# Optimization experiments

Hardware: AMD Instinct MI355X
Metric: run time of the kernel (lower is better)

The kernel has to match this reference:

```python
import jax, jax.numpy as jnp
import numpy as np
from jax import lax

B, M, N = 4096, 306, 984
LAMBDA = 0.1
MAX_ITER = 50


def setup_inputs() -> dict:
    key = jax.random.key(0)
    k1, k2, k3, k4 = jax.random.split(key, 4)
    return {
        "r_real": jax.random.normal(k1, (B, M), dtype=jnp.float32),
        "r_imag": jax.random.normal(k2, (B, M), dtype=jnp.float32),
        # phi buffer: torch.randn(M, N, dtype=complex64) -> real/imag each ~N(0, 1/2)?
        # torch.randn(complex64) draws real & imag each from N(0, 1/sqrt(2)^2)=N(0,0.5).
        "phi_real": jax.random.normal(k3, (M, N), dtype=jnp.float32) * np.float32(1.0 / np.sqrt(2.0)),
        "phi_imag": jax.random.normal(k4, (M, N), dtype=jnp.float32) * np.float32(1.0 / np.sqrt(2.0)),
    }


def reference(r_real, r_imag, phi_real, phi_imag):
    phi = (phi_real + 1j * phi_imag).astype(jnp.complex64)          # [M, N]
    r = (r_real + 1j * r_imag).astype(jnp.complex64)                # [B, M]
    # step_size = 1 / ||phi||_2^2  (spectral norm squared)
    step = (1.0 / jnp.linalg.norm(phi, ord=2) ** 2).real.astype(jnp.float32)
    thresh = (LAMBDA * step).astype(jnp.float32)
    phi_c = jnp.conj(phi)

    def body(w, _):
        # error = w @ phi.T - r : [B, M]
        error = jnp.einsum("bn,mn->bm", w, phi) - r
        # gradient = error @ conj(phi) : [B, N]
        grad = jnp.einsum("bm,mn->bn", error, phi_c)
        w_next = w - step * grad
        w_mag = jnp.abs(w_next)
        new_mag = jax.nn.relu(w_mag - thresh)
        # polar(new_mag, angle(w_next))
        w_new = (new_mag * jnp.exp(1j * jnp.angle(w_next))).astype(jnp.complex64)
        return w_new, None

    w0 = jnp.zeros((r.shape[0], N), dtype=jnp.complex64)
    w, _ = lax.scan(body, w0, None, length=MAX_ITER)
    return jnp.abs(w).astype(jnp.float32)
```

## Files before the change

kernel.cpp:

```cpp
#include <hip/hip_runtime.h>
#include <math.h>

#define Bb 4096
#define Mm 306
#define Nn 984
#define NCP 1024
#define KA 2048
#define ITERS 50
#define KSQ 9

typedef _Float16 f16x8 __attribute__((ext_vector_type(8)));
typedef float f32x16 __attribute__((ext_vector_type(16)));

__device__ __forceinline__ void cmac(float2& c, const float2 a, const float2 b) {
    c.x = fmaf(a.x, b.x, c.x);
    c.x = fmaf(-a.y, b.y, c.x);
    c.y = fmaf(a.x, b.y, c.y);
    c.y = fmaf(a.y, b.x, c.y);
}

__device__ __forceinline__ unsigned short f16bits(float v) {
    union { _Float16 h; unsigned short u; } cv;
    cv.h = (_Float16)v;
    return cv.u;
}
__device__ __forceinline__ float f16lo(unsigned int u) {
    union { unsigned short s; _Float16 h; } cv; cv.s = (unsigned short)(u & 0xffffu);
    return (float)cv.h;
}
__device__ __forceinline__ float f16hi(unsigned int u) {
    union { unsigned short s; _Float16 h; } cv; cv.s = (unsigned short)(u >> 16);
    return (float)cv.h;
}

__device__ __forceinline__ void load_lds16(const void* g, void* l) {
    __builtin_amdgcn_global_load_lds((const __attribute__((address_space(1))) void*)g,
                                     (__attribute__((address_space(3))) void*)l, 16, 0, 0);
}

__device__ __forceinline__ size_t swzA(int b, int c) {
    return ((size_t)(((b >> 7) * 32 + (c >> 5)) * 1024 + ((c >> 2) & 7) * 128 + (b & 127))) * 4 + (c & 3);
}
__device__ __forceinline__ size_t swzB(int jr, int q) {
    return ((size_t)(((jr >> 7) * 32 + (q >> 5)) * 1024 + ((q >> 2) & 7) * 128 + (jr & 127))) * 4 + (q & 3);
}
__device__ __forceinline__ size_t swzA2(int b, int c) {
    return ((size_t)(((b >> 7) * 10 + (c >> 5)) * 1024 + ((c >> 2) & 7) * 128 + (b & 127))) * 4 + (c & 3);
}
__device__ __forceinline__ size_t swzB2(int jr, int q) {
    return ((size_t)(((jr >> 7) * 10 + (q >> 5)) * 1024 + ((q >> 2) & 7) * 128 + (jr & 127))) * 4 + (q & 3);
}

__global__ void gram_kernel(const float* __restrict__ pr, const float* __restrict__ pi,
                            float2* __restrict__ G) {
    __shared__ float2 As[32][33];
    __shared__ float2 Bs[32][33];
    int tx = threadIdx.x, ty = threadIdx.y;
    int t = ty * 16 + tx;
    int i0 = blockIdx.y * 32, j0 = blockIdx.x * 32;
    int zs = blockIdx.z * 246;
    int ze = zs + 246 < Nn ? zs + 246 : Nn;
    float2 acc[2][2] = {};
    for (int k0 = zs; k0 < ze; k0 += 32) {
        #pragma unroll
        for (int rep = 0; rep < 4; ++rep) {
            int idx = t + rep * 256;
            int rr = idx >> 5, cc = idx & 31;
            int gk = k0 + cc;
            int gi = i0 + rr, gj = j0 + rr;
            float2 a = make_float2(0.f, 0.f), b = make_float2(0.f, 0.f);
            if (gk < ze) {
                if (gi < Mm) a = make_float2(pr[(size_t)gi * Nn + gk], pi[(size_t)gi * Nn + gk]);
                if (gj < Mm) b = make_float2(pr[(size_t)gj * Nn + gk], pi[(size_t)gj * Nn + gk]);
            }
            As[rr][cc] = a; Bs[rr][cc] = b;
        }
        __syncthreads();
        #pragma unroll 8
        for (int kk = 0; kk < 32; ++kk) {
            float2 a0 = As[ty * 2][kk], a1 = As[ty * 2 + 1][kk];
            float2 b0 = Bs[tx * 2][kk], b1 = Bs[tx * 2 + 1][kk];
            #define GMAC(qq, aa, bb) \
                qq.x = fmaf(aa.x, bb.x, qq.x); qq.x = fmaf(aa.y, bb.y, qq.x); \
                qq.y = fmaf(aa.y, bb.x, qq.y); qq.y = fmaf(-aa.x, bb.y, qq.y);
            GMAC(acc[0][0], a0, b0) GMAC(acc[0][1], a0, b1)
            GMAC(acc[1][0], a1, b0) GMAC(acc[1][1], a1, b1)
            #undef GMAC
        }
        __syncthreads();
    }
    #pragma unroll
    for (int i = 0; i < 2; ++i) {
        int gi = i0 + ty * 2 + i;
        #pragma unroll
        for (int j = 0; j < 2; ++j) {
            int gj = j0 + tx * 2 + j;
            if (gi < Mm && gj < Mm) {
                atomicAdd(&G[gi * Mm + gj].x, acc[i][j].x);
                atomicAdd(&G[gi * Mm + gj].y, acc[i][j].y);
            }
        }
    }
}

__global__ void frob_kernel(const float2* __restrict__ H, float* __restrict__ slot, int n) {
    int idx = blockIdx.x * blockDim.x + threadIdx.x;
    int stride = gridDim.x * blockDim.x;
    float s = 0.f;
    for (int i = idx; i < n; i += stride) {
        float2 v = H[i];
        s = fmaf(v.x, v.x, s);
        s = fmaf(v.y, v.y, s);
    }
    #pragma unroll
    for (int o = 32; o > 0; o >>= 1) s += __shfl_down(s, o, 64);
    __shared__ float wsum[4];
    int lane = threadIdx.x & 63, wv = threadIdx.x >> 6;
    if (lane == 0) wsum[wv] = s;
    __syncthreads();
    if (threadIdx.x == 0) atomicAdd(slot, wsum[0] + wsum[1] + wsum[2] + wsum[3]);
}

__global__ void sqmm_kernel(const float2* __restrict__ A, float2* __restrict__ C,
                            const float* __restrict__ fslot) {
    __shared__ float2 As[32][33];
    __shared__ float2 Bs[32][33];
    float inv = 1.0f / fslot[0];
    int tx = threadIdx.x, ty = threadIdx.y;
    int t = ty * 16 + tx;
    int r0 = blockIdx.y * 32, c0 = blockIdx.x * 32;
    int zs = blockIdx.z * 80;
    int ze = zs + 80 < Mm ? zs + 80 : Mm;
    float2 acc[2][2] = {};
    for (int k0 = zs; k0 < ze; k0 += 32) {
        #pragma unroll
        for (int i = 0; i < 4; ++i) {
            int idx = t + i * 256;
            int rr = idx >> 5, cc = idx & 31;
            int gr = r0 + rr, gk = k0 + cc;
            As[rr][cc] = (gr < Mm && gk < ze) ? A[gr * Mm + gk] : make_float2(0.f, 0.f);
            int gk2 = k0 + rr, gc = c0 + cc;
            Bs[rr][cc] = (gk2 < ze && gc < Mm) ? A[gk2 * Mm + gc] : make_float2(0.f, 0.f);
        }
        __syncthreads();
        #pragma unroll 8
        for (int kk = 0; kk < 32; ++kk) {
            float2 a0 = As[ty * 2][kk], a1 = As[ty * 2 + 1][kk];
            float2 b0 = Bs[kk][tx * 2], b1 = Bs[kk][tx * 2 + 1];
            cmac(acc[0][0], a0, b0); cmac(acc[0][1], a0, b1);
            cmac(acc[1][0], a1, b0); cmac(acc[1][1], a1, b1);
        }
        __syncthreads();
    }
    #pragma unroll
    for (int i = 0; i < 2; ++i) {
        int gr = r0 + ty * 2 + i;
        #pragma unroll
        for (int j = 0; j < 2; ++j) {
            int gc = c0 + tx * 2 + j;
            if (gr < Mm && gc < Mm) {
                atomicAdd(&C[gr * Mm + gc].x, acc[i][j].x * inv);
                atomicAdd(&C[gr * Mm + gc].y, acc[i][j].y * inv);
            }
        }
    }
}

__global__ void rayleigh_kernel(const float2* __restrict__ H, const float2* __restrict__ G,
                                float* __restrict__ sc) {
    __shared__ float2 v[Mm];
    __shared__ float rn[320], rd[320];
    int t = threadIdx.x;
    if (t < Mm) {
        float2 s = make_float2(0.f, 0.f);
        for (int j = 0; j < Mm; ++j) { float2 h = H[t * Mm + j]; s.x += h.x; s.y += h.y; }
        v[t] = s;
    }
    __syncthreads();
    float num = 0.f, den = 0.f;
    if (t < Mm) {
        float2 u = make_float2(0.f, 0.f);
        for (int k = 0; k < Mm; ++k) {
            float2 g = G[k * Mm + t];
            float2 vk = v[k];
            u.x = fmaf(g.x, vk.x, u.x); u.x = fmaf(g.y, vk.y, u.x);
            u.y = fmaf(g.x, vk.y, u.y); u.y = fmaf(-g.y, vk.x, u.y);
        }
        float2 vt = v[t];
        num = vt.x * u.x + vt.y * u.y;
        den = vt.x * vt.x + vt.y * vt.y;
    }
    rn[t] = num; rd[t] = den;
    __syncthreads();
    if (t == 0) {
        float sn = 0.f, sd = 0.f;
        for (int i = 0; i < 320; ++i) { sn += rn[i]; sd += rd[i]; }
        float lam = sn / sd;
        float step = 1.0f / lam;
        sc[0] = step;
        sc[1] = 0.1f * step;
    }
}

__global__ void qpack_kernel(const float* __restrict__ pr, const float* __restrict__ pi,
                             unsigned int* __restrict__ Bu, const float* __restrict__ sc) {
    __shared__ float2 Pn[16][33];
    __shared__ float2 Pc[16][33];
    float nstep = -sc[0];
    int t = threadIdx.x;
    int tx = t & 15, ty = t >> 4;
    int n0 = blockIdx.x * 32, c0 = blockIdx.y * 32;
    float2 q[2][2] = {};
    for (int m0 = 0; m0 < Mm; m0 += 16) {
        #pragma unroll
        for (int rep = 0; rep < 2; ++rep) {
            int idx = t + rep * 256;
            int mm = idx >> 5, col = idx & 31;
            int gm = m0 + mm;
            float2 a = make_float2(0.f, 0.f), b = make_float2(0.f, 0.f);
            if (gm < Mm) {
                if (n0 + col < Nn) a = make_float2(pr[(size_t)gm * Nn + n0 + col], pi[(size_t)gm * Nn + n0 + col]);
                if (c0 + col < Nn) b = make_float2(pr[(size_t)gm * Nn + c0 + col], pi[(size_t)gm * Nn + c0 + col]);
            }
            Pn[mm][col] = a; Pc[mm][col] = b;
        }
        __syncthreads();
        #pragma unroll
        for (int mm = 0; mm < 16; ++mm) {
            float2 a0 = Pn[mm][ty * 2], a1 = Pn[mm][ty * 2 + 1];
            float2 b0 = Pc[mm][tx * 2], b1 = Pc[mm][tx * 2 + 1];
            #define QMAC(qq, aa, bb) \
                qq.x = fmaf(aa.x, bb.x, qq.x); qq.x = fmaf(aa.y, bb.y, qq.x); \
                qq.y = fmaf(aa.y, bb.x, qq.y); qq.y = fmaf(-aa.x, bb.y, qq.y);
            QMAC(q[0][0], a0, b0) QMAC(q[0][1], a0, b1)
            QMAC(q[1][0], a1, b0) QMAC(q[1][1], a1, b1)
            #undef QMAC
        }
        __syncthreads();
    }
    #pragma unroll
    for (int i = 0; i < 2; ++i) {
        int n = n0 + ty * 2 + i;
        #pragma unroll
        for (int j = 0; j < 2; ++j) {
            int c = c0 + tx * 2 + j;
            if (n < Nn && c < Nn) {
                float MR = fmaf(nstep, q[i][j].x, (n == c) ? 1.0f : 0.0f);
                float MI = nstep * q[i][j].y;
                unsigned short hR = f16bits(MR);
                unsigned short hI = f16bits(MI);
                unsigned short nhI = hI ^ 0x8000u;
                int jr = ((c >> 5) * 64) + (c & 31);
                Bu[swzB(jr, n)]      = (unsigned)hR | ((unsigned)nhI << 16);
                Bu[swzB(jr + 32, n)] = (unsigned)hI | ((unsigned)hR << 16);
            }
        }
    }
}

__global__ void rpack_kernel(const float* __restrict__ rr, const float* __restrict__ ri,
                             unsigned int* __restrict__ rp16) {
    int b = blockIdx.x * 256 + threadIdx.x;
    int m = blockIdx.y;
    rp16[swzA2(b, m)] = (unsigned)f16bits(rr[(size_t)b * Mm + m]) |
                        ((unsigned)f16bits(ri[(size_t)b * Mm + m]) << 16);
}

__global__ void ppack2_kernel(const float* __restrict__ pr, const float* __restrict__ pi,
                              unsigned int* __restrict__ B2u, const float* __restrict__ sc) {
    int n = blockIdx.x * 256 + threadIdx.x;
    int m = blockIdx.y;
    if (n >= Nn) return;
    float s = sc[0];
    float xr = pr[(size_t)m * Nn + n], xi = pi[(size_t)m * Nn + n];
    unsigned short x = f16bits(-s * xr), y = f16bits(-s * xi);
    int jr2 = ((n >> 5) * 64) + (n & 31);
    B2u[swzB2(jr2, m)]      = (unsigned)x | ((unsigned)y << 16);
    B2u[swzB2(jr2 + 32, m)] = (unsigned)(y ^ 0x8000u) | ((unsigned)x << 16);
}

__global__ __launch_bounds__(256, 2) void rphi_mfma_kernel(
    const _Float16* __restrict__ rp16, const _Float16* __restrict__ B2,
    unsigned int* __restrict__ rph16) {
    __shared__ _Float16 As[8192];
    __shared__ _Float16 Bs[8192];
    int tid = threadIdx.x;
    int lane = tid & 63, wv = tid >> 6;
    int wm = wv & 1, wn = wv >> 1;
    int bblk = blockIdx.x, nblk = blockIdx.y;
    int l31 = lane & 31, lh = lane >> 5;

    f32x16 acc[2][2] = {};

    for (int kt = 0; kt < 10; ++kt) {
        #pragma unroll
        for (int c = 0; c < 4; ++c) {
            int u = c * 256 + tid;
            const char* ga = (const char*)rp16 + (((size_t)(bblk * 10 + kt)) * 1024 + u) * 16;
            load_lds16(ga, &As[(size_t)(c * 256 + wv * 64) * 8]);
            const char* gb = (const char*)B2 + (((size_t)(nblk * 10 + kt)) * 1024 + u) * 16;
            load_lds16(gb, &Bs[(size_t)(c * 256 + wv * 64) * 8]);
        }
        __syncthreads();
        #pragma unroll
        for (int s = 0; s < 4; ++s) {
            int kq = s * 2 + lh;
            f16x8 af[2], bfr[2];
            #pragma unroll
            for (int mt = 0; mt < 2; ++mt)
                af[mt] = *reinterpret_cast<const f16x8*>(
                    &As[(size_t)(kq * 128 + wm * 64 + mt * 32 + l31) * 8]);
            #pragma unroll
            for (int nt = 0; nt < 2; ++nt)
                bfr[nt] = *reinterpret_cast<const f16x8*>(
                    &Bs[(size_t)(kq * 128 + wn * 64 + nt * 32 + l31) * 8]);
            #pragma unroll
            for (int mt = 0; mt < 2; ++mt)
                #pragma unroll
                for (int nt = 0; nt < 2; ++nt)
                    acc[mt][nt] = __builtin_amdgcn_mfma_f32_32x32x16_f16(af[mt], bfr[nt], acc[mt][nt], 0, 0, 0);
        }
        __syncthreads();
    }

    int b0 = bblk * 128;
    int c = nblk * 64 + wn * 32 + l31;
    #pragma unroll
    for (int mt = 0; mt < 2; ++mt) {
        #pragma unroll
        for (int reg = 0; reg < 16; ++reg) {
            int row = b0 + wm * 64 + mt * 32 + ((reg & 3) + 8 * (reg >> 2) + 4 * lh);
            rph16[(size_t)row * NCP + c] =
                (unsigned)f16bits(-acc[mt][0][reg]) | ((unsigned)f16bits(-acc[mt][1][reg]) << 16);
        }
    }
}

__global__ __launch_bounds__(512) void ista9_kernel(
    const _Float16* __restrict__ wfi, const _Float16* __restrict__ Bq,
    unsigned int* __restrict__ wfo,
    const unsigned int* __restrict__ rph16,
    const float* __restrict__ sc, float* __restrict__ out, int last) {
    __shared__ _Float16 As0[8192], As1[8192];
    __shared__ _Float16 Bs0[2][8192], Bs1[2][8192];
    int tid = threadIdx.x;
    int lane = tid & 63, wv = tid >> 6;
    int wm = wv >> 2, wn = wv & 3;
    int id = blockIdx.x;
    int bblk = id >> 3;
    int nb2 = id & 7;
    int l31 = lane & 31, lh = lane >> 5;
    int slab = wn >> 1, chg = wn & 1;

    f32x16 acc[2][2] = {};

    const char* gA  = (const char*)wfi + (size_t)bblk * 32 * 1024 * 16;
    const char* gB0 = (const char*)Bq + (size_t)(nb2 * 2 + 0) * 32 * 1024 * 16;
    const char* gB1 = (const char*)Bq + (size_t)(nb2 * 2 + 1) * 32 * 1024 * 16;

    #define STAGE9(kt, Ad, Bd)                                                        \
        {                                                                             \
            _Float16* Ap = (Ad);                                                      \
            _Float16* Bp0 = &(Bd)[0][0];                                              \
            _Float16* Bp1 = &(Bd)[1][0];                                              \
            _Pragma("unroll")                                                         \
            for (int cc = 0; cc < 2; ++cc) {                                          \
                int u = cc * 512 + tid;                                               \
                size_t ldst = (size_t)(cc * 512 + wv * 64) * 8;                       \
                load_lds16(gA + ((size_t)(kt) * 1024 + u) * 16, &Ap[ldst]);           \
                load_lds16(gB0 + ((size_t)(kt) * 1024 + u) * 16, &Bp0[ldst]);         \
                load_lds16(gB1 + ((size_t)(kt) * 1024 + u) * 16, &Bp1[ldst]);         \
            }                                                                         \
        }

    #define COMPUTE9(Asrc, Bsrc)                                                      \
        {                                                                             \
            _Pragma("unroll")                                                         \
            for (int s = 0; s < 4; ++s) {                                             \
                int kq = s * 2 + lh;                                                  \
                f16x8 af[2], bf[2];                                                   \
                _Pragma("unroll")                                                     \
                for (int mt = 0; mt < 2; ++mt)                                        \
                    af[mt] = *reinterpret_cast<const f16x8*>(                         \
                        &(Asrc)[(size_t)(kq * 128 + wm * 64 + mt * 32 + l31) * 8]);   \
                _Pragma("unroll")                                                     \
                for (int nt = 0; nt < 2; ++nt)                                        \
                    bf[nt] = *reinterpret_cast<const f16x8*>(                         \
                        &(Bsrc)[slab][(size_t)(kq * 128 + chg * 64 + nt * 32 + l31) * 8]); \
                _Pragma("unroll")                                                     \
                for (int mt = 0; mt < 2; ++mt)                                        \
                    _Pragma("unroll")                                                 \
                    for (int nt = 0; nt < 2; ++nt)                                    \
                        acc[mt][nt] = __builtin_amdgcn_mfma_f32_32x32x16_f16(         \
                            af[mt], bf[nt], acc[mt][nt], 0, 0, 0);                    \
            }                                                                         \
        }

    STAGE9(0, As0, Bs0);
    for (int kt = 0; kt < 32; kt += 2) {
        STAGE9(kt + 1, As1, Bs1);
        asm volatile("s_waitcnt vmcnt(6)" ::: "memory");
        __builtin_amdgcn_s_barrier();
        COMPUTE9(As0, Bs0);
        __builtin_amdgcn_s_barrier();
        STAGE9(kt + 2, As0, Bs0);
        asm volatile("s_waitcnt vmcnt(6)" ::: "memory");
        __builtin_amdgcn_s_barrier();
        COMPUTE9(As1, Bs1);
        __builtin_amdgcn_s_barrier();
    }
    #undef STAGE9
    #undef COMPUTE9

    float thr = sc[1];
    int b0 = bblk * 128;
    int c = nb2 * 128 + wn * 32 + l31;
    #pragma unroll
    for (int mt = 0; mt < 2; ++mt) {
        #pragma unroll
        for (int reg = 0; reg < 16; ++reg) {
            int row = b0 + wm * 64 + mt * 32 + ((reg & 3) + 8 * (reg >> 2) + 4 * lh);
            unsigned int ru = rph16[(size_t)row * NCP + c];
            float zr = acc[mt][0][reg] + f16lo(ru);
            float zi = acc[mt][1][reg] + f16hi(ru);
            float mag = sqrtf(zr * zr + zi * zi);
            float nm = mag - thr;
            float f = (nm > 0.f) ? (nm / mag) : 0.f;
            wfo[swzA(row, c)] = (unsigned)f16bits(zr * f) | ((unsigned)f16bits(zi * f) << 16);
            if (last && c < Nn) out[(size_t)row * Nn + c] = fmaxf(nm, 0.f);
        }
    }
}

extern "C" void kernel_launch(void* const* d_in, const int* in_sizes, int n_in,
                              void* d_out, int out_size, void* d_ws, size_t ws_size,
                              hipStream_t stream) {
    const float* rr = (const float*)d_in[0];
    const float* ri = (const float*)d_in[1];
    const float* pr = (const float*)d_in[2];
    const float* pi = (const float*)d_in[3];
    float* out = (float*)d_out;

    char* ws = (char*)d_ws;
    size_t off = 0;
    _Float16* wf0 = (_Float16*)(ws + off); off += (size_t)Bb * KA * sizeof(_Float16);
    _Float16* wf1 = (_Float16*)(ws + off); off += (size_t)Bb * KA * sizeof(_Float16);
    _Float16* Bq  = (_Float16*)(ws + off); off += (size_t)2048 * 2048 * sizeof(_Float16);
    unsigned int* rph16 = (unsigned int*)(ws + off); off += (size_t)Bb * NCP * 4;
    _Float16* rp16 = (_Float16*)(ws + off); off += (size_t)Bb * 640 * sizeof(_Float16);
    _Float16* B2  = (_Float16*)(ws + off); off += (size_t)2048 * 640 * sizeof(_Float16);
    float2* G = (float2*)(ws + off);     off += (size_t)Mm * Mm * sizeof(float2);
    float2* H1 = (float2*)(ws + off);    off += (size_t)Mm * Mm * sizeof(float2);
    float2* H2 = (float2*)(ws + off);    off += (size_t)Mm * Mm * sizeof(float2);
    float* slots = (float*)(ws + off);   off += 64 * sizeof(float);
    float* sc = slots + 32;

    (void)hipMemsetAsync(wf0, 0, (size_t)Bb * KA * sizeof(_Float16), stream);
    (void)hipMemsetAsync(Bq, 0, (size_t)2048 * 2048 * sizeof(_Float16), stream);
    (void)hipMemsetAsync(rp16, 0, (size_t)Bb * 640 * sizeof(_Float16), stream);
    (void)hipMemsetAsync(B2, 0, (size_t)2048 * 640 * sizeof(_Float16), stream);
    (void)hipMemsetAsync(slots, 0, 64 * sizeof(float), stream);
    (void)hipMemsetAsync(G, 0, (size_t)Mm * Mm * sizeof(float2), stream);

    gram_kernel<<<dim3(10, 10, 4), dim3(16, 16), 0, stream>>>(pr, pi, G);
    float2* bufs[2] = { H1, H2 };
    const float2* src = G;
    for (int s = 0; s < KSQ; ++s) {
        frob_kernel<<<128, 256, 0, stream>>>(src, slots + s, Mm * Mm);
        float2* dst = bufs[s & 1];
        (void)hipMemsetAsync(dst, 0, (size_t)Mm * Mm * sizeof(float2), stream);
        sqmm_kernel<<<dim3(10, 10, 4), dim3(16, 16), 0, stream>>>(src, dst, slots + s);
        src = dst;
    }
    rayleigh_kernel<<<1, 320, 0, stream>>>(src, G, sc);

    qpack_kernel<<<dim3(31, 31), 256, 0, stream>>>(pr, pi, (unsigned int*)Bq, sc);
    rpack_kernel<<<dim3(16, Mm), 256, 0, stream>>>(rr, ri, (unsigned int*)rp16);
    ppack2_kernel<<<dim3(4, Mm), 256, 0, stream>>>(pr, pi, (unsigned int*)B2, sc);
    rphi_mfma_kernel<<<dim3(32, 16), 256, 0, stream>>>(rp16, B2, rph16);

    _Float16* wbuf[2] = { wf0, wf1 };
    for (int it = 0; it < ITERS; ++it) {
        ista9_kernel<<<256, 512, 0, stream>>>(
            wbuf[it & 1], Bq, (unsigned int*)wbuf[(it + 1) & 1], rph16, sc, out,
            it == ITERS - 1 ? 1 : 0);
    }
}
```

Before: 2.992 ms.

## Parallelize Rayleigh quotient, fuse memset into frob, widen qpack tiles, remap ista blocks

Replaces the single-block Rayleigh kernel with two grid-wide reduction kernels plus a tiny finalize kernel, removing a serial single-block bottleneck. The per-step memset of the squaring destination is folded into the Frobenius-norm kernel, and qpack computes 2x4 outputs per thread over 64-wide column tiles. The ISTA kernel's block-id to (batch block, column block) mapping is permuted so concurrently running blocks share B operand data in cache. These are mostly setup-phase costs; the block remap affects the 50-iteration main loop.

```diff
diff --git a/kernel.cpp b/kernel.cpp
--- a/kernel.cpp
+++ b/kernel.cpp
@@ -103,7 +103,8 @@
     }
 }
 
-__global__ void frob_kernel(const float2* __restrict__ H, float* __restrict__ slot, int n) {
+__global__ void frobz_kernel(const float2* __restrict__ H, float* __restrict__ slot,
+                             float2* __restrict__ dst, int n) {
     int idx = blockIdx.x * blockDim.x + threadIdx.x;
     int stride = gridDim.x * blockDim.x;
     float s = 0.f;
@@ -111,6 +112,7 @@
         float2 v = H[i];
         s = fmaf(v.x, v.x, s);
         s = fmaf(v.y, v.y, s);
+        dst[i] = make_float2(0.f, 0.f);
     }
     #pragma unroll
     for (int o = 32; o > 0; o >>= 1) s += __shfl_down(s, o, 64);
@@ -166,74 +168,97 @@
     }
 }
 
-__global__ void rayleigh_kernel(const float2* __restrict__ H, const float2* __restrict__ G,
-                                float* __restrict__ sc) {
-    __shared__ float2 v[Mm];
-    __shared__ float rn[320], rd[320];
-    int t = threadIdx.x;
-    if (t < Mm) {
-        float2 s = make_float2(0.f, 0.f);
-        for (int j = 0; j < Mm; ++j) { float2 h = H[t * Mm + j]; s.x += h.x; s.y += h.y; }
-        v[t] = s;
-    }
+__global__ void ray1_kernel(const float2* __restrict__ H, float2* __restrict__ v) {
+    int t = blockIdx.x;
+    int k = threadIdx.x;
+    float sx = 0.f, sy = 0.f;
+    for (int j = k; j < Mm; j += 256) {
+        float2 h = H[(size_t)t * Mm + j];
+        sx += h.x; sy += h.y;
+    }
+    #pragma unroll
+    for (int o = 32; o > 0; o >>= 1) { sx += __shfl_down(sx, o, 64); sy += __shfl_down(sy, o, 64); }
+    __shared__ float wx[4], wy[4];
+    int lane = k & 63, wv = k >> 6;
+    if (lane == 0) { wx[wv] = sx; wy[wv] = sy; }
     __syncthreads();
-    float num = 0.f, den = 0.f;
-    if (t < Mm) {
-        float2 u = make_float2(0.f, 0.f);
-        for (int k = 0; k < Mm; ++k) {
-            float2 g = G[k * Mm + t];
-            float2 vk = v[k];
-            u.x = fmaf(g.x, vk.x, u.x); u.x = fmaf(g.y, vk.y, u.x);
-            u.y = fmaf(g.x, vk.y, u.y); u.y = fmaf(-g.y, vk.x, u.y);
-        }
+    if (k == 0) v[t] = make_float2(wx[0] + wx[1] + wx[2] + wx[3],
+                                   wy[0] + wy[1] + wy[2] + wy[3]);
+}
+
+__global__ void ray2_kernel(const float2* __restrict__ G, const float2* __restrict__ v,
+                            float* __restrict__ slots) {
+    int t = blockIdx.x;
+    int k0 = threadIdx.x;
+    float ux = 0.f, uy = 0.f;
+    for (int k = k0; k < Mm; k += 256) {
+        float2 g = G[(size_t)k * Mm + t];
+        float2 vk = v[k];
+        ux = fmaf(g.x, vk.x, ux); ux = fmaf(g.y, vk.y, ux);
+        uy = fmaf(g.x, vk.y, uy); uy = fmaf(-g.y, vk.x, uy);
+    }
+    #pragma unroll
+    for (int o = 32; o > 0; o >>= 1) { ux += __shfl_down(ux, o, 64); uy += __shfl_down(uy, o, 64); }
+    __shared__ float wx[4], wy[4];
+    int lane = k0 & 63, wv = k0 >> 6;
+    if (lane == 0) { wx[wv] = ux; wy[wv] = uy; }
+    __syncthreads();
+    if (k0 == 0) {
+        float sux = wx[0] + wx[1] + wx[2] + wx[3];
+        float suy = wy[0] + wy[1] + wy[2] + wy[3];
         float2 vt = v[t];
-        num = vt.x * u.x + vt.y * u.y;
-        den = vt.x * vt.x + vt.y * vt.y;
-    }
-    rn[t] = num; rd[t] = den;
-    __syncthreads();
-    if (t == 0) {
-        float sn = 0.f, sd = 0.f;
-        for (int i = 0; i < 320; ++i) { sn += rn[i]; sd += rd[i]; }
-        float lam = sn / sd;
-        float step = 1.0f / lam;
-        sc[0] = step;
-        sc[1] = 0.1f * step;
-    }
+        atomicAdd(&slots[16], vt.x * sux + vt.y * suy);
+        atomicAdd(&slots[17], vt.x * vt.x + vt.y * vt.y);
+    }
+}
+
+__global__ void ray3_kernel(const float* __restrict__ slots, float* __restrict__ sc) {
+    float step = slots[17] / slots[16];
+    sc[0] = step;
+    sc[1] = 0.1f * step;
 }
 
 __global__ void qpack_kernel(const float* __restrict__ pr, const float* __restrict__ pi,
                              unsigned int* __restrict__ Bu, const float* __restrict__ sc) {
     __shared__ float2 Pn[16][33];
-    __shared__ float2 Pc[16][33];
+    __shared__ float2 Pc[16][65];
     float nstep = -sc[0];
     int t = threadIdx.x;
     int tx = t & 15, ty = t >> 4;
-    int n0 = blockIdx.x * 32, c0 = blockIdx.y * 32;
-    float2 q[2][2] = {};
+    int n0 = blockIdx.x * 32, c0 = blockIdx.y * 64;
+    float2 q[2][4] = {};
     for (int m0 = 0; m0 < Mm; m0 += 16) {
         #pragma unroll
-        for (int rep = 0; rep < 2; ++rep) {
+        for (int rep = 0; rep < 6; ++rep) {
             int idx = t + rep * 256;
-            int mm = idx >> 5, col = idx & 31;
-            int gm = m0 + mm;
-            float2 a = make_float2(0.f, 0.f), b = make_float2(0.f, 0.f);
-            if (gm < Mm) {
-                if (n0 + col < Nn) a = make_float2(pr[(size_t)gm * Nn + n0 + col], pi[(size_t)gm * Nn + n0 + col]);
-                if (c0 + col < Nn) b = make_float2(pr[(size_t)gm * Nn + c0 + col], pi[(size_t)gm * Nn + c0 + col]);
+            if (idx < 512) {
+                int mm = idx >> 5, col = idx & 31;
+                int gm = m0 + mm;
+                float2 a = make_float2(0.f, 0.f);
+                if (gm < Mm && n0 + col < Nn)
+                    a = make_float2(pr[(size_t)gm * Nn + n0 + col], pi[(size_t)gm * Nn + n0 + col]);
+                Pn[mm][col] = a;
+            } else {
+                int idx2 = idx - 512;
+                int mm = idx2 >> 6, col = idx2 & 63;
+                int gm = m0 + mm;
+                float2 b = make_float2(0.f, 0.f);
+                if (gm < Mm && c0 + col < Nn)
+                    b = make_float2(pr[(size_t)gm * Nn + c0 + col], pi[(size_t)gm * Nn + c0 + col]);
+                Pc[mm][col] = b;
             }
-            Pn[mm][col] = a; Pc[mm][col] = b;
         }
         __syncthreads();
         #pragma unroll
         for (int mm = 0; mm < 16; ++mm) {
             float2 a0 = Pn[mm][ty * 2], a1 = Pn[mm][ty * 2 + 1];
-            float2 b0 = Pc[mm][tx * 2], b1 = Pc[mm][tx * 2 + 1];
+            float2 b0 = Pc[mm][tx * 4], b1 = Pc[mm][tx * 4 + 1];
+            float2 b2 = Pc[mm][tx * 4 + 2], b3 = Pc[mm][tx * 4 + 3];
             #define QMAC(qq, aa, bb) \
                 qq.x = fmaf(aa.x, bb.x, qq.x); qq.x = fmaf(aa.y, bb.y, qq.x); \
                 qq.y = fmaf(aa.y, bb.x, qq.y); qq.y = fmaf(-aa.x, bb.y, qq.y);
-            QMAC(q[0][0], a0, b0) QMAC(q[0][1], a0, b1)
-            QMAC(q[1][0], a1, b0) QMAC(q[1][1], a1, b1)
+            QMAC(q[0][0], a0, b0) QMAC(q[0][1], a0, b1) QMAC(q[0][2], a0, b2) QMAC(q[0][3], a0, b3)
+            QMAC(q[1][0], a1, b0) QMAC(q[1][1], a1, b1) QMAC(q[1][2], a1, b2) QMAC(q[1][3], a1, b3)
             #undef QMAC
         }
         __syncthreads();
@@ -242,8 +267,8 @@
     for (int i = 0; i < 2; ++i) {
         int n = n0 + ty * 2 + i;
         #pragma unroll
-        for (int j = 0; j < 2; ++j) {
-            int c = c0 + tx * 2 + j;
+        for (int j = 0; j < 4; ++j) {
+            int c = c0 + tx * 4 + j;
             if (n < Nn && c < Nn) {
                 float MR = fmaf(nstep, q[i][j].x, (n == c) ? 1.0f : 0.0f);
                 float MI = nstep * q[i][j].y;
@@ -347,8 +372,10 @@
     int lane = tid & 63, wv = tid >> 6;
     int wm = wv >> 2, wn = wv & 3;
     int id = blockIdx.x;
-    int bblk = id >> 3;
-    int nb2 = id & 7;
+    int x = id & 7;
+    int n = id >> 3;
+    int bblk = (x & 3) * 8 + (n & 7);
+    int nb2  = (x >> 2) * 4 + (n >> 3);
     int l31 = lane & 31, lh = lane >> 5;
     int slab = wn >> 1, chg = wn & 1;
 
@@ -452,6 +479,7 @@
     float2* G = (float2*)(ws + off);     off += (size_t)Mm * Mm * sizeof(float2);
     float2* H1 = (float2*)(ws + off);    off += (size_t)Mm * Mm * sizeof(float2);
     float2* H2 = (float2*)(ws + off);    off += (size_t)Mm * Mm * sizeof(float2);
+    float2* vvec = (float2*)(ws + off);  off += (size_t)Mm * sizeof(float2);
     float* slots = (float*)(ws + off);   off += 64 * sizeof(float);
     float* sc = slots + 32;
 
@@ -466,15 +494,16 @@
     float2* bufs[2] = { H1, H2 };
     const float2* src = G;
     for (int s = 0; s < KSQ; ++s) {
-        frob_kernel<<<128, 256, 0, stream>>>(src, slots + s, Mm * Mm);
         float2* dst = bufs[s & 1];
-        (void)hipMemsetAsync(dst, 0, (size_t)Mm * Mm * sizeof(float2), stream);
+        frobz_kernel<<<128, 256, 0, stream>>>(src, slots + s, dst, Mm * Mm);
         sqmm_kernel<<<dim3(10, 10, 4), dim3(16, 16), 0, stream>>>(src, dst, slots + s);
         src = dst;
     }
-    rayleigh_kernel<<<1, 320, 0, stream>>>(src, G, sc);
-
-    qpack_kernel<<<dim3(31, 31), 256, 0, stream>>>(pr, pi, (unsigned int*)Bq, sc);
+    ray1_kernel<<<Mm, 256, 0, stream>>>(src, vvec);
+    ray2_kernel<<<Mm, 256, 0, stream>>>(G, vvec, slots);
+    ray3_kernel<<<1, 1, 0, stream>>>(slots, sc);
+
+    qpack_kernel<<<dim3(31, 16), 256, 0, stream>>>(pr, pi, (unsigned int*)Bq, sc);
     rpack_kernel<<<dim3(16, Mm), 256, 0, stream>>>(rr, ri, (unsigned int*)rp16);
     ppack2_kernel<<<dim3(4, Mm), 256, 0, stream>>>(pr, pi, (unsigned int*)B2, sc);
     rphi_mfma_kernel<<<dim3(32, 16), 256, 0, stream>>>(rp16, B2, rph16);
```

New measurement: 2.882 ms. 3.7% less time.
